# Kernel optimization log

Hardware: AMD Instinct MI355X
Metric: run time of the kernel (lower is better)

The kernel has to match this reference:

```python
import jax, jax.numpy as jnp
import numpy as np

B, C, H, W = 2, 256, 48, 48
NH = 8
HD = C // NH  # 32
T = H * W    # 2304


def setup_inputs() -> dict:
    keys = jax.random.split(jax.random.key(0), 16)
    s = lambda fan: 1.0 / np.sqrt(fan)
    x = jax.random.normal(keys[0], (B, C, H, W), jnp.float32)
    wq = jax.random.normal(keys[1], (C, C), jnp.float32) * s(C)
    bq = jax.random.normal(keys[2], (C,), jnp.float32) * 0.01
    wk = jax.random.normal(keys[3], (C, C), jnp.float32) * s(C)
    bk = jax.random.normal(keys[4], (C,), jnp.float32) * 0.01
    wv = jax.random.normal(keys[5], (C, C), jnp.float32) * s(C)
    bv = jax.random.normal(keys[6], (C,), jnp.float32) * 0.01
    wo = jax.random.normal(keys[7], (C, C), jnp.float32) * s(C)
    bo = jax.random.normal(keys[8], (C,), jnp.float32) * 0.01
    gamma1 = jnp.ones((C,), jnp.float32)
    beta1 = jnp.zeros((C,), jnp.float32)
    w1 = jax.random.normal(keys[9], (4 * C, C), jnp.float32) * s(C)
    bf1 = jax.random.normal(keys[10], (4 * C,), jnp.float32) * 0.01
    w2 = jax.random.normal(keys[11], (C, 4 * C), jnp.float32) * s(4 * C)
    bf2 = jax.random.normal(keys[12], (C,), jnp.float32) * 0.01
    gamma2 = jnp.ones((C,), jnp.float32)
    beta2 = jnp.zeros((C,), jnp.float32)
    return dict(x=x, wq=wq, bq=bq, wk=wk, bk=bk, wv=wv, bv=bv, wo=wo, bo=bo,
                gamma1=gamma1, beta1=beta1, w1=w1, bf1=bf1, w2=w2, bf2=bf2,
                gamma2=gamma2, beta2=beta2)


def group_norm1(x, gamma, beta, eps=1e-5):
    # GroupNorm(1, C): normalize over (C, H, W) per sample, per-channel affine.
    mu = jnp.mean(x, axis=(1, 2, 3), keepdims=True)
    var = jnp.mean((x - mu) ** 2, axis=(1, 2, 3), keepdims=True)
    xn = (x - mu) * jax.lax.rsqrt(var + eps)
    return xn * gamma[None, :, None, None] + beta[None, :, None, None]


def reference(x, wq, bq, wk, bk, wv, bv, wo, bo, gamma1, beta1,
              w1, bf1, w2, bf2, gamma2, beta2):
    b, c, h, w = x.shape
    t = h * w
    xt = x.reshape(b, c, t).transpose(0, 2, 1)  # [b, t, c]
    # 1x1 conv == per-token linear
    def heads(y):
        return y.reshape(b, t, NH, HD).transpose(0, 2, 1, 3)  # [b, nh, t, hd]
    q = heads(xt @ wq.T + bq)
    k = heads(xt @ wk.T + bk)
    v = heads(xt @ wv.T + bv)
    # flash SDPA runs in fp16 with fp32 accumulation
    q16 = q.astype(jnp.float16)
    k16 = k.astype(jnp.float16)
    v16 = v.astype(jnp.float16)
    scale = 1.0 / np.sqrt(HD)
    scores = jnp.einsum('bhqd,bhkd->bhqk', q16.astype(jnp.float32),
                        k16.astype(jnp.float32)) * scale
    attn = jax.nn.softmax(scores, axis=-1)
    out = jnp.einsum('bhqk,bhkd->bhqd', attn,
                     v16.astype(jnp.float32)).astype(jnp.float16)
    # remove component along normalized v (fp16, like torch code)
    vn = v16 / jnp.maximum(
        jnp.sqrt(jnp.sum(v16 * v16, axis=-1, keepdims=True)),
        jnp.float16(1e-12))
    out = out - jnp.sum(out * vn, axis=-1, keepdims=True) * vn
    out = out.astype(x.dtype)
    out = out.transpose(0, 2, 1, 3).reshape(b, t, c)  # [b, t, c]
    out = out @ wo.T + bo
    out = out.transpose(0, 2, 1).reshape(b, c, h, w)
    x1 = group_norm1(x + out, gamma1, beta1)
    # FFN: 1x1 conv -> relu -> 1x1 conv, per token
    x1t = x1.reshape(b, c, t).transpose(0, 2, 1)  # [b, t, c]
    hdn = jax.nn.relu(x1t @ w1.T + bf1)
    ffn = (hdn @ w2.T + bf2).transpose(0, 2, 1).reshape(b, c, h, w)
    x2 = group_norm1(x1 + ffn, gamma2, beta2)
    return x2
```

## Files before the change

### kernel.cpp

```cpp
#include <hip/hip_runtime.h>
#include <hip/hip_fp16.h>

typedef _Float16 f16x8 __attribute__((ext_vector_type(8)));
typedef float f32x4 __attribute__((ext_vector_type(4)));

namespace {

constexpr int B = 2, C = 256, T = 2304, F = 1024, NH = 8, HD = 32;
constexpr int BH = B * NH;
constexpr int NCHUNK = 4;
constexpr int CHUNK = T / NCHUNK;
constexpr float C2 = 0.17677669529663687f * 1.4426950408889634f;
constexpr float INV_N = 1.0f / (float)(C * T);

constexpr size_t N_WQKV = (size_t)3 * C * C;
constexpr size_t N_WO   = (size_t)C * C;
constexpr size_t N_W1   = (size_t)F * C;
constexpr size_t N_W2   = (size_t)C * F;
constexpr size_t N_WALL = N_WQKV + N_WO + N_W1 + N_W2;

constexpr size_t OFF_QKV  = 0;
constexpr size_t SZ_QKV   = (size_t)B * 3 * C * T * 2;
constexpr size_t OFF_AO   = OFF_QKV + SZ_QKV;
constexpr size_t SZ_AO    = (size_t)B * C * T * 2;
constexpr size_t OFF_X1   = OFF_AO + SZ_AO;
constexpr size_t SZ_X1    = (size_t)B * C * T * 4;
constexpr size_t OFF_PART = OFF_X1 + SZ_X1;
constexpr size_t SZ_OP    = (size_t)NCHUNK * BH * HD * T * 2;
constexpr size_t SZ_MP    = (size_t)NCHUNK * BH * T * 4;
constexpr size_t OFF_OP   = OFF_PART;
constexpr size_t OFF_MP   = OFF_OP + SZ_OP;
constexpr size_t OFF_LP   = OFF_MP + SZ_MP;
constexpr size_t SZ_H16   = (size_t)B * F * T * 2;
constexpr size_t SZ_PART  = SZ_OP + 2 * SZ_MP;
constexpr size_t SZ_UNION = SZ_PART > SZ_H16 ? SZ_PART : SZ_H16;
constexpr size_t OFF_H16  = OFF_PART;
constexpr size_t OFF_W16  = OFF_PART + SZ_UNION;
constexpr size_t OFF_BQKV = OFF_W16 + N_WALL * 2;
constexpr size_t OFF_STATS = OFF_BQKV + (size_t)3 * C * 4;

}

__global__ __launch_bounds__(256)
void convert_weights(const float* __restrict__ wq, const float* __restrict__ wk,
                     const float* __restrict__ wv, const float* __restrict__ wo,
                     const float* __restrict__ w1, const float* __restrict__ w2,
                     const float* __restrict__ bq, const float* __restrict__ bk,
                     const float* __restrict__ bv,
                     _Float16* __restrict__ w16, float* __restrict__ bqkv,
                     float* __restrict__ stats)
{
  const size_t tid = (size_t)blockIdx.x * 256 + threadIdx.x;
  if (tid < 8) stats[tid] = 0.f;
  if (tid < 3 * C)
    bqkv[tid] = tid < C ? bq[tid] : (tid < 2 * C ? bk[tid - C] : bv[tid - 2 * C]);
  for (size_t i = tid; i < N_WALL; i += (size_t)gridDim.x * 256) {
    float v;
    if      (i < 65536)  v = wq[i];
    else if (i < 131072) v = wk[i - 65536];
    else if (i < 196608) v = wv[i - 131072];
    else if (i < 262144) v = wo[i - 196608];
    else if (i < 524288) v = w1[i - 262144];
    else                 v = w2[i - 524288];
    w16[i] = (_Float16)v;
  }
}

template<bool RELU, bool RES, bool GNIN, bool GNRES, bool STATS,
         typename InT, typename OutT>
__global__ __launch_bounds__(256)
void gemm_mfma(const _Float16* __restrict__ W, const InT* __restrict__ X,
               const float* __restrict__ bias, const float* __restrict__ res,
               OutT* __restrict__ out, int CO, int K,
               const float* __restrict__ stats_in,
               const float* __restrict__ gamma, const float* __restrict__ beta,
               float* __restrict__ stats_out)
{
  const int b   = blockIdx.z;
  const int co0 = blockIdx.y * 64;
  const int t0  = blockIdx.x * 64;
  const int tid = threadIdx.x;
  const int wid = tid >> 6, lane = tid & 63;
  const int g = lane >> 4, lo = lane & 15;
  const int wm = wid & 1, wn = wid >> 1;

  __shared__ f16x8 xs[4][64];
  __shared__ float gs[256], bs[256];
  __shared__ float red[8];

  float mu = 0.f, rsig = 0.f;
  if (GNIN || GNRES) {
    const float s1 = stats_in[b * 2], s2 = stats_in[b * 2 + 1];
    mu = s1 * INV_N;
    rsig = rsqrtf(s2 * INV_N - mu * mu + 1e-5f);
  }
  if (GNIN) { gs[tid] = gamma[tid]; bs[tid] = beta[tid]; }

  const f32x4 z4 = {0.f, 0.f, 0.f, 0.f};
  f32x4 acc00 = z4, acc01 = z4, acc10 = z4, acc11 = z4;

  const int st = tid & 63;
  const int kp = tid >> 6;
  const InT* Xp = X + (size_t)b * K * T + t0 + st;
  const _Float16* Wp = W + (size_t)(co0 + wm * 32 + lo) * K + 8 * g;

  float xr[8];
#pragma unroll
  for (int j = 0; j < 8; ++j) xr[j] = (float)Xp[(size_t)(kp * 8 + j) * T];
  f16x8 af0 = *(const f16x8*)(Wp);
  f16x8 af1 = *(const f16x8*)(Wp + (size_t)16 * K);

  __syncthreads();

  for (int k0 = 0; k0 < K; k0 += 32) {
    f16x8 wv_;
#pragma unroll
    for (int j = 0; j < 8; ++j) {
      float v = xr[j];
      if (GNIN) { const int k = k0 + kp * 8 + j; v = (v - mu) * rsig * gs[k] + bs[k]; }
      wv_[j] = (_Float16)v;
    }
    xs[kp][st] = wv_;

    const int k1 = (k0 + 32 < K) ? k0 + 32 : k0;
    float xr2[8];
#pragma unroll
    for (int j = 0; j < 8; ++j) xr2[j] = (float)Xp[(size_t)(k1 + kp * 8 + j) * T];
    const f16x8 afn0 = *(const f16x8*)(Wp + (size_t)k1);
    const f16x8 afn1 = *(const f16x8*)(Wp + (size_t)16 * K + k1);

    __syncthreads();
    const f16x8 bf0 = xs[g][wn * 32 + lo];
    const f16x8 bf1 = xs[g][wn * 32 + 16 + lo];
    acc00 = __builtin_amdgcn_mfma_f32_16x16x32_f16(af0, bf0, acc00, 0, 0, 0);
    acc01 = __builtin_amdgcn_mfma_f32_16x16x32_f16(af0, bf1, acc01, 0, 0, 0);
    acc10 = __builtin_amdgcn_mfma_f32_16x16x32_f16(af1, bf0, acc10, 0, 0, 0);
    acc11 = __builtin_amdgcn_mfma_f32_16x16x32_f16(af1, bf1, acc11, 0, 0, 0);
    __syncthreads();

#pragma unroll
    for (int j = 0; j < 8; ++j) xr[j] = xr2[j];
    af0 = afn0;
    af1 = afn1;
  }

  float s = 0.f, ss = 0.f;
  const size_t obase = ((size_t)b * CO + co0 + wm * 32) * T + t0 + wn * 32 + lo;
  const float* resb = res + obase;
  OutT* outb = out + obase;
  const f32x4 accs[2][2] = {{acc00, acc01}, {acc10, acc11}};
#pragma unroll
  for (int mi = 0; mi < 2; ++mi) {
#pragma unroll
    for (int r = 0; r < 4; ++r) {
      const int row = mi * 16 + 4 * g + r;
      const int co = co0 + wm * 32 + row;
      const float bi = bias[co];
      float gm = 0.f, bt = 0.f;
      if (GNRES) { gm = gamma[co]; bt = beta[co]; }
#pragma unroll
      for (int ni = 0; ni < 2; ++ni) {
        float v = accs[mi][ni][r] + bi;
        if (RES) {
          float rv = resb[(size_t)row * T + ni * 16];
          if (GNRES) rv = (rv - mu) * rsig * gm + bt;
          v += rv;
        }
        if (RELU) v = fmaxf(v, 0.f);
        outb[(size_t)row * T + ni * 16] = (OutT)v;
        if (STATS) { s += v; ss = fmaf(v, v, ss); }
      }
    }
  }

  if (STATS) {
#pragma unroll
    for (int off = 32; off > 0; off >>= 1) {
      s  += __shfl_down(s, off);
      ss += __shfl_down(ss, off);
    }
    if (lane == 0) { red[wid] = s; red[4 + wid] = ss; }
    __syncthreads();
    if (tid == 0) {
      atomicAdd(&stats_out[b * 2],     red[0] + red[1] + red[2] + red[3]);
      atomicAdd(&stats_out[b * 2 + 1], red[4] + red[5] + red[6] + red[7]);
    }
  }
}

__global__ __launch_bounds__(256)
void attn_mfma(const _Float16* __restrict__ qkv, _Float16* __restrict__ opart,
               float* __restrict__ mpart, float* __restrict__ lpart)
{
  const int tid  = threadIdx.x;
  const int wid  = tid >> 6;
  const int lane = tid & 63;
  const int g    = lane >> 4;
  const int lo   = lane & 15;
  const int chunk = blockIdx.y;
  const int bh   = blockIdx.z;
  const int b    = bh >> 3, h = bh & 7;
  const int tq   = blockIdx.x * 64 + wid * 16 + lo;
  const size_t qb = ((size_t)b * 3 * C + h * HD) * T;
  const size_t kb = qb + (size_t)C * T;
  const size_t vb = qb + (size_t)2 * C * T;

  __shared__ _Float16 kt[64][36];
  __shared__ _Float16 pl[4][16][72];

  f16x8 qf;
#pragma unroll
  for (int j = 0; j < 8; ++j)
    qf[j] = (_Float16)((float)qkv[qb + (size_t)(8 * g + j) * T + tq] * C2);

  const f32x4 zero4 = {0.f, 0.f, 0.f, 0.f};
  f32x4 oa[2] = {zero4, zero4};
  float m = -1e30f, l = 0.f;

  for (int it = 0; it < CHUNK / 64; ++it) {
    const int tk0 = chunk * CHUNK + it * 64;
    __syncthreads();
    {
      const int t = tid & 63;
      const int dp0 = tid >> 6;
#pragma unroll
      for (int dd = 0; dd < 4; ++dd) {
        const int d = (dp0 * 4 + dd) * 2;
        const ushort klo = *(const ushort*)(qkv + kb + (size_t)d * T + tk0 + t);
        const ushort khi = *(const ushort*)(qkv + kb + (size_t)(d + 1) * T + tk0 + t);
        *(uint*)&kt[t][d] = (uint)klo | ((uint)khi << 16);
      }
    }
    __syncthreads();

    f16x8 vfr[2][2];
#pragma unroll
    for (int c2 = 0; c2 < 2; ++c2)
#pragma unroll
      for (int dt = 0; dt < 2; ++dt)
        vfr[c2][dt] = *(const f16x8*)(qkv + vb + (size_t)(dt * 16 + lo) * T +
                                      tk0 + c2 * 32 + 8 * g);

    f32x4 s4[4];
#pragma unroll
    for (int mt = 0; mt < 4; ++mt) {
      union { f16x8 v; uint2 u[2]; } kf;
      const _Float16* kr = &kt[mt * 16 + lo][8 * g];
      kf.u[0] = *(const uint2*)(kr);
      kf.u[1] = *(const uint2*)(kr + 4);
      s4[mt] = __builtin_amdgcn_mfma_f32_16x16x32_f16(kf.v, qf, zero4, 0, 0, 0);
    }
    float rmax = -1e30f;
#pragma unroll
    for (int mt = 0; mt < 4; ++mt) {
      const float m01 = fmaxf(s4[mt][0], s4[mt][1]);
      const float m23 = fmaxf(s4[mt][2], s4[mt][3]);
      rmax = fmaxf(rmax, fmaxf(m01, m23));
    }
    rmax = fmaxf(rmax, __shfl_xor(rmax, 16));
    rmax = fmaxf(rmax, __shfl_xor(rmax, 32));
    const float mn = fmaxf(m, rmax);
    const float fsc = __builtin_amdgcn_exp2f(m - mn);
    m = mn;
    float p[4][4];
    float psum = 0.f;
#pragma unroll
    for (int mt = 0; mt < 4; ++mt)
#pragma unroll
      for (int r = 0; r < 4; ++r) {
        p[mt][r] = __builtin_amdgcn_exp2f(s4[mt][r] - mn);
        psum += p[mt][r];
      }
    psum += __shfl_xor(psum, 16);
    psum += __shfl_xor(psum, 32);
    l = l * fsc + psum;
#pragma unroll
    for (int dt = 0; dt < 2; ++dt)
#pragma unroll
      for (int r = 0; r < 4; ++r) oa[dt][r] *= fsc;

#pragma unroll
    for (int mt = 0; mt < 4; ++mt) {
      union { _Float16 e[4]; uint2 u2; } pw;
#pragma unroll
      for (int r = 0; r < 4; ++r) pw.e[r] = (_Float16)p[mt][r];
      *(uint2*)&pl[wid][lo][16 * mt + 4 * g] = pw.u2;
    }
#pragma unroll
    for (int c2 = 0; c2 < 2; ++c2) {
      const f16x8 pbv = *(const f16x8*)&pl[wid][lo][c2 * 32 + 8 * g];
#pragma unroll
      for (int dt = 0; dt < 2; ++dt)
        oa[dt] = __builtin_amdgcn_mfma_f32_16x16x32_f16(vfr[c2][dt], pbv, oa[dt], 0, 0, 0);
    }
  }

  const float invL = 1.f / l;
  const size_t ob = (size_t)(chunk * BH + bh) * HD * T;
#pragma unroll
  for (int dt = 0; dt < 2; ++dt)
#pragma unroll
    for (int r = 0; r < 4; ++r)
      opart[ob + (size_t)(dt * 16 + 4 * g + r) * T + tq] =
          (_Float16)(oa[dt][r] * invL);
  if (g == 0) {
    const size_t pb = (size_t)(chunk * BH + bh) * T + tq;
    mpart[pb] = m;
    lpart[pb] = l;
  }
}

__global__ __launch_bounds__(64)
void attn_combine(const _Float16* __restrict__ opart, const float* __restrict__ mpart,
                  const float* __restrict__ lpart, const _Float16* __restrict__ qkv,
                  _Float16* __restrict__ AOh)
{
  const int q  = blockIdx.x * 64 + threadIdx.x;
  const int bh = blockIdx.y;
  const int b  = bh >> 3, h = bh & 7;
  float mv[NCHUNK], lv[NCHUNK];
  float M = -1e30f;
#pragma unroll
  for (int c = 0; c < NCHUNK; ++c) {
    const size_t pb = (size_t)(c * BH + bh) * T + q;
    mv[c] = mpart[pb];
    lv[c] = lpart[pb];
    M = fmaxf(M, mv[c]);
  }
  float L = 0.f;
  float wc[NCHUNK];
#pragma unroll
  for (int c = 0; c < NCHUNK; ++c) {
    wc[c] = __builtin_amdgcn_exp2f(mv[c] - M) * lv[c];
    L += wc[c];
  }
  const float inv = 1.f / L;
#pragma unroll
  for (int c = 0; c < NCHUNK; ++c) wc[c] *= inv;

  float o[HD];
#pragma unroll
  for (int d = 0; d < HD; ++d) o[d] = 0.f;
#pragma unroll
  for (int c = 0; c < NCHUNK; ++c) {
    const size_t ob = (size_t)(c * BH + bh) * HD * T + q;
#pragma unroll
    for (int d = 0; d < HD; ++d)
      o[d] = fmaf(wc[c], (float)opart[ob + (size_t)d * T], o[d]);
  }

  const size_t vbase = ((size_t)b * 3 * C + 2 * C + h * HD) * T + q;
  float vv[HD], nrm2 = 0.f;
#pragma unroll
  for (int d = 0; d < HD; ++d) {
    vv[d] = (float)qkv[vbase + (size_t)d * T];
    nrm2 = fmaf(vv[d], vv[d], nrm2);
  }
  const float nrm = fmaxf(sqrtf(nrm2), 1e-12f);
  float dot = 0.f;
  float o16[HD], vn[HD];
#pragma unroll
  for (int d = 0; d < HD; ++d) {
    o16[d] = (float)(_Float16)(o[d]);
    vn[d]  = (float)(_Float16)(vv[d] / nrm);
    dot = fmaf(o16[d], vn[d], dot);
  }
  const size_t ab = ((size_t)b * C + h * HD) * T + q;
#pragma unroll
  for (int d = 0; d < HD; ++d)
    AOh[ab + (size_t)d * T] = (_Float16)(o16[d] - dot * vn[d]);
}

__global__ __launch_bounds__(256)
void gn_norm(const float* __restrict__ Y, const float* __restrict__ stats,
             const float* __restrict__ gamma, const float* __restrict__ beta,
             float* __restrict__ O)
{
  const int i = blockIdx.x * 256 + threadIdx.x;
  const int b = i / (C * T);
  const int c = (i / T) & (C - 1);
  const float mu  = stats[b * 2] * INV_N;
  const float var = stats[b * 2 + 1] * INV_N - mu * mu;
  const float r = rsqrtf(var + 1e-5f);
  O[i] = (Y[i] - mu) * r * gamma[c] + beta[c];
}

extern "C" void kernel_launch(void* const* d_in, const int* in_sizes, int n_in,
                              void* d_out, int out_size, void* d_ws, size_t ws_size,
                              hipStream_t stream)
{
  const float* x      = (const float*)d_in[0];
  const float* wq     = (const float*)d_in[1];
  const float* bq     = (const float*)d_in[2];
  const float* wk     = (const float*)d_in[3];
  const float* bk     = (const float*)d_in[4];
  const float* wv     = (const float*)d_in[5];
  const float* bv     = (const float*)d_in[6];
  const float* wo     = (const float*)d_in[7];
  const float* bo     = (const float*)d_in[8];
  const float* gamma1 = (const float*)d_in[9];
  const float* beta1  = (const float*)d_in[10];
  const float* w1     = (const float*)d_in[11];
  const float* bf1    = (const float*)d_in[12];
  const float* w2     = (const float*)d_in[13];
  const float* bf2    = (const float*)d_in[14];
  const float* gamma2 = (const float*)d_in[15];
  const float* beta2  = (const float*)d_in[16];

  char* ws = (char*)d_ws;
  _Float16* qkv16 = (_Float16*)(ws + OFF_QKV);
  _Float16* ao16  = (_Float16*)(ws + OFF_AO);
  float*    x1    = (float*)(ws + OFF_X1);
  _Float16* opart = (_Float16*)(ws + OFF_OP);
  float*    mpart = (float*)(ws + OFF_MP);
  float*    lpart = (float*)(ws + OFF_LP);
  _Float16* h16   = (_Float16*)(ws + OFF_H16);
  _Float16* w16   = (_Float16*)(ws + OFF_W16);
  float*    bqkv  = (float*)(ws + OFF_BQKV);
  float*    stats = (float*)(ws + OFF_STATS);
  float*    out   = (float*)d_out;

  const _Float16* wqkv16 = w16;
  const _Float16* wo16   = w16 + N_WQKV;
  const _Float16* w116   = w16 + N_WQKV + N_WO;
  const _Float16* w216   = w16 + N_WQKV + N_WO + N_W1;

  const dim3 blk256(256);

  convert_weights<<<768, blk256, 0, stream>>>(wq, wk, wv, wo, w1, w2, bq, bk, bv,
                                              w16, bqkv, stats);

  gemm_mfma<false, false, false, false, false, float, _Float16>
      <<<dim3(36, 12, 2), blk256, 0, stream>>>(
          wqkv16, x, bqkv, nullptr, qkv16, 3 * C, C, nullptr, nullptr, nullptr, nullptr);

  attn_mfma<<<dim3(T / 64, NCHUNK, BH), blk256, 0, stream>>>(qkv16, opart, mpart, lpart);
  attn_combine<<<dim3(T / 64, BH), dim3(64), 0, stream>>>(opart, mpart, lpart, qkv16, ao16);

  gemm_mfma<false, true, false, false, true, _Float16, float>
      <<<dim3(36, 4, 2), blk256, 0, stream>>>(
          wo16, ao16, bo, x, x1, C, C, nullptr, nullptr, nullptr, stats);

  gemm_mfma<true, false, true, false, false, float, _Float16>
      <<<dim3(36, 16, 2), blk256, 0, stream>>>(
          w116, x1, bf1, nullptr, h16, F, C, stats, gamma1, beta1, nullptr);

  gemm_mfma<false, true, false, true, true, _Float16, float>
      <<<dim3(36, 4, 2), blk256, 0, stream>>>(
          w216, h16, bf2, x1, out, C, F, stats, gamma1, beta1, stats + 4);

  gn_norm<<<dim3(4608), blk256, 0, stream>>>(out, stats + 4, gamma2, beta2, out);
}
```

Baseline: 144.8 us.

## Store K token-major from QKV GEMM, drop attention LDS transpose, raise split count

The QKV projection GEMM now writes the K section in a per-head token-major layout, so the attention kernel can load K fragments straight from global memory. This removes the shared-memory K transpose and its two barriers per iteration. The key dimension is also split into 6 chunks instead of 4 for more parallelism, and the attention loop is unrolled by 2. In exchange, the register double-buffered prefetch in the GEMM main loop is removed, which may expose more load latency in every GEMM. The combine kernel must also handle more partial results.

```diff
diff --git a/kernel.cpp b/kernel.cpp
--- a/kernel.cpp
+++ b/kernel.cpp
@@ -8,7 +8,7 @@
 
 constexpr int B = 2, C = 256, T = 2304, F = 1024, NH = 8, HD = 32;
 constexpr int BH = B * NH;
-constexpr int NCHUNK = 4;
+constexpr int NCHUNK = 6;
 constexpr int CHUNK = T / NCHUNK;
 constexpr float C2 = 0.17677669529663687f * 1.4426950408889634f;
 constexpr float INV_N = 1.0f / (float)(C * T);
@@ -66,7 +66,7 @@
   }
 }
 
-template<bool RELU, bool RES, bool GNIN, bool GNRES, bool STATS,
+template<bool RELU, bool RES, bool GNIN, bool GNRES, bool STATS, bool KT,
          typename InT, typename OutT>
 __global__ __launch_bounds__(256)
 void gemm_mfma(const _Float16* __restrict__ W, const InT* __restrict__ X,
@@ -104,32 +104,21 @@
   const InT* Xp = X + (size_t)b * K * T + t0 + st;
   const _Float16* Wp = W + (size_t)(co0 + wm * 32 + lo) * K + 8 * g;
 
-  float xr[8];
-#pragma unroll
-  for (int j = 0; j < 8; ++j) xr[j] = (float)Xp[(size_t)(kp * 8 + j) * T];
-  f16x8 af0 = *(const f16x8*)(Wp);
-  f16x8 af1 = *(const f16x8*)(Wp + (size_t)16 * K);
-
   __syncthreads();
 
   for (int k0 = 0; k0 < K; k0 += 32) {
     f16x8 wv_;
 #pragma unroll
     for (int j = 0; j < 8; ++j) {
-      float v = xr[j];
-      if (GNIN) { const int k = k0 + kp * 8 + j; v = (v - mu) * rsig * gs[k] + bs[k]; }
+      const int k = k0 + kp * 8 + j;
+      float v = (float)Xp[(size_t)k * T];
+      if (GNIN) v = (v - mu) * rsig * gs[k] + bs[k];
       wv_[j] = (_Float16)v;
     }
     xs[kp][st] = wv_;
-
-    const int k1 = (k0 + 32 < K) ? k0 + 32 : k0;
-    float xr2[8];
-#pragma unroll
-    for (int j = 0; j < 8; ++j) xr2[j] = (float)Xp[(size_t)(k1 + kp * 8 + j) * T];
-    const f16x8 afn0 = *(const f16x8*)(Wp + (size_t)k1);
-    const f16x8 afn1 = *(const f16x8*)(Wp + (size_t)16 * K + k1);
-
     __syncthreads();
+    const f16x8 af0 = *(const f16x8*)(Wp + (size_t)k0);
+    const f16x8 af1 = *(const f16x8*)(Wp + (size_t)16 * K + k0);
     const f16x8 bf0 = xs[g][wn * 32 + lo];
     const f16x8 bf1 = xs[g][wn * 32 + 16 + lo];
     acc00 = __builtin_amdgcn_mfma_f32_16x16x32_f16(af0, bf0, acc00, 0, 0, 0);
@@ -137,18 +126,37 @@
     acc10 = __builtin_amdgcn_mfma_f32_16x16x32_f16(af1, bf0, acc10, 0, 0, 0);
     acc11 = __builtin_amdgcn_mfma_f32_16x16x32_f16(af1, bf1, acc11, 0, 0, 0);
     __syncthreads();
-
-#pragma unroll
-    for (int j = 0; j < 8; ++j) xr[j] = xr2[j];
-    af0 = afn0;
-    af1 = afn1;
+  }
+
+  const f32x4 accs[2][2] = {{acc00, acc01}, {acc10, acc11}};
+
+  if constexpr (KT) {
+    if (co0 >= 256 && co0 < 512) {
+      const int h = ((co0 - 256) >> 5) + wm;
+      _Float16* kbase = (_Float16*)out + ((size_t)b * 3 * C + C) * T +
+                        (size_t)h * T * 32;
+      const int t = t0 + wn * 32 + lo;
+#pragma unroll
+      for (int mi = 0; mi < 2; ++mi) {
+#pragma unroll
+        for (int ni = 0; ni < 2; ++ni) {
+          union { _Float16 e[4]; uint2 u; } pk;
+#pragma unroll
+          for (int r = 0; r < 4; ++r) {
+            const int co = co0 + wm * 32 + mi * 16 + 4 * g + r;
+            pk.e[r] = (_Float16)(accs[mi][ni][r] + bias[co]);
+          }
+          *(uint2*)(kbase + (size_t)(t + ni * 16) * 32 + mi * 16 + 4 * g) = pk.u;
+        }
+      }
+      return;
+    }
   }
 
   float s = 0.f, ss = 0.f;
   const size_t obase = ((size_t)b * CO + co0 + wm * 32) * T + t0 + wn * 32 + lo;
   const float* resb = res + obase;
   OutT* outb = out + obase;
-  const f32x4 accs[2][2] = {{acc00, acc01}, {acc10, acc11}};
 #pragma unroll
   for (int mi = 0; mi < 2; ++mi) {
 #pragma unroll
@@ -202,10 +210,9 @@
   const int b    = bh >> 3, h = bh & 7;
   const int tq   = blockIdx.x * 64 + wid * 16 + lo;
   const size_t qb = ((size_t)b * 3 * C + h * HD) * T;
-  const size_t kb = qb + (size_t)C * T;
-  const size_t vb = qb + (size_t)2 * C * T;
-
-  __shared__ _Float16 kt[64][36];
+  const size_t vb = ((size_t)b * 3 * C + 2 * C + h * HD) * T;
+  const _Float16* ktp = qkv + ((size_t)b * 3 * C + C) * T + (size_t)h * T * 32;
+
   __shared__ _Float16 pl[4][16][72];
 
   f16x8 qf;
@@ -217,22 +224,14 @@
   f32x4 oa[2] = {zero4, zero4};
   float m = -1e30f, l = 0.f;
 
+#pragma unroll 2
   for (int it = 0; it < CHUNK / 64; ++it) {
     const int tk0 = chunk * CHUNK + it * 64;
-    __syncthreads();
-    {
-      const int t = tid & 63;
-      const int dp0 = tid >> 6;
-#pragma unroll
-      for (int dd = 0; dd < 4; ++dd) {
-        const int d = (dp0 * 4 + dd) * 2;
-        const ushort klo = *(const ushort*)(qkv + kb + (size_t)d * T + tk0 + t);
-        const ushort khi = *(const ushort*)(qkv + kb + (size_t)(d + 1) * T + tk0 + t);
-        *(uint*)&kt[t][d] = (uint)klo | ((uint)khi << 16);
-      }
-    }
-    __syncthreads();
-
+
+    f16x8 kf[4];
+#pragma unroll
+    for (int mt = 0; mt < 4; ++mt)
+      kf[mt] = *(const f16x8*)(ktp + (size_t)(tk0 + mt * 16 + lo) * 32 + 8 * g);
     f16x8 vfr[2][2];
 #pragma unroll
     for (int c2 = 0; c2 < 2; ++c2)
@@ -243,13 +242,9 @@
 
     f32x4 s4[4];
 #pragma unroll
-    for (int mt = 0; mt < 4; ++mt) {
-      union { f16x8 v; uint2 u[2]; } kf;
-      const _Float16* kr = &kt[mt * 16 + lo][8 * g];
-      kf.u[0] = *(const uint2*)(kr);
-      kf.u[1] = *(const uint2*)(kr + 4);
-      s4[mt] = __builtin_amdgcn_mfma_f32_16x16x32_f16(kf.v, qf, zero4, 0, 0, 0);
-    }
+    for (int mt = 0; mt < 4; ++mt)
+      s4[mt] = __builtin_amdgcn_mfma_f32_16x16x32_f16(kf[mt], qf, zero4, 0, 0, 0);
+
     float rmax = -1e30f;
 #pragma unroll
     for (int mt = 0; mt < 4; ++mt) {
@@ -430,22 +425,22 @@
   convert_weights<<<768, blk256, 0, stream>>>(wq, wk, wv, wo, w1, w2, bq, bk, bv,
                                               w16, bqkv, stats);
 
-  gemm_mfma<false, false, false, false, false, float, _Float16>
+  gemm_mfma<false, false, false, false, false, true, float, _Float16>
       <<<dim3(36, 12, 2), blk256, 0, stream>>>(
           wqkv16, x, bqkv, nullptr, qkv16, 3 * C, C, nullptr, nullptr, nullptr, nullptr);
 
   attn_mfma<<<dim3(T / 64, NCHUNK, BH), blk256, 0, stream>>>(qkv16, opart, mpart, lpart);
   attn_combine<<<dim3(T / 64, BH), dim3(64), 0, stream>>>(opart, mpart, lpart, qkv16, ao16);
 
-  gemm_mfma<false, true, false, false, true, _Float16, float>
+  gemm_mfma<false, true, false, false, true, false, _Float16, float>
       <<<dim3(36, 4, 2), blk256, 0, stream>>>(
           wo16, ao16, bo, x, x1, C, C, nullptr, nullptr, nullptr, stats);
 
-  gemm_mfma<true, false, true, false, false, float, _Float16>
+  gemm_mfma<true, false, true, false, false, false, float, _Float16>
       <<<dim3(36, 16, 2), blk256, 0, stream>>>(
           w116, x1, bf1, nullptr, h16, F, C, stats, gamma1, beta1, nullptr);
 
-  gemm_mfma<false, true, false, true, true, _Float16, float>
+  gemm_mfma<false, true, false, true, true, false, _Float16, float>
       <<<dim3(36, 4, 2), blk256, 0, stream>>>(
           w216, h16, bf2, x1, out, C, F, stats, gamma1, beta1, stats + 4);
 
```

Result: slower. 197.2 us (+36.1%).
